# Performance work log

Hardware: AMD Instinct MI355X
Metric: run time of the kernel (lower is better)

The kernel has to match this reference:

```python
import jax, jax.numpy as jnp
import numpy as np

P_DROP = 0.25
DROP_KEY_SEED = 42  # fixed seed makes dropout deterministic for baseline comparison


def setup_inputs() -> dict:
    key = jax.random.key(0)
    k1, k2, k3, k4 = jax.random.split(key, 4)
    B, S, D, DV = 16, 2048, 64, 512
    x1 = jax.random.normal(k1, (B, S, D), dtype=jnp.float32)   # queries [B,S,64]
    m = jax.random.normal(k2, (D, DV), dtype=jnp.float32)      # [64,512]
    n = jax.random.normal(k3, (S, DV), dtype=jnp.float32)      # [S,512]
    q = jax.random.normal(k4, (S, DV), dtype=jnp.float32)      # values [S,512]
    return {"x1": x1, "m": m, "n": n, "q": q}


def reference(x1, m, n, q):
    scale = jnp.float32(1.0 / 64.0)  # hard-coded in original (not 1/sqrt(d))
    kT = jnp.matmul(m, n.T)                        # matmul5: [64, S]
    scores = jnp.matmul(x1, kT) * scale            # [B, S, S]
    probs = jax.nn.softmax(scores, axis=-1)        # softmax over last dim
    keep = jax.random.bernoulli(jax.random.key(DROP_KEY_SEED), 1.0 - P_DROP, probs.shape)
    probs = jnp.where(keep, probs / (1.0 - P_DROP), jnp.float32(0.0))  # dropout (train mode)
    return jnp.matmul(probs, q)                    # [B, S, DV]
```

## Files before the change

kernel.cpp:

```cpp
#include <hip/hip_runtime.h>
#include <hip/hip_bf16.h>


typedef short  s8v __attribute__((ext_vector_type(8)));
typedef float  f4v __attribute__((ext_vector_type(4)));

__device__ __forceinline__ unsigned short f2bf(float f) {
  unsigned int u = __float_as_uint(f);
  u += 0x7fffu + ((u >> 16) & 1u);
  return (unsigned short)(u >> 16);
}
__device__ __forceinline__ unsigned int pack_bf2(float a, float b) {
  __hip_bfloat162 h = __float22bfloat162_rn(float2{a, b});
  unsigned int u;
  __builtin_memcpy(&u, &h, 4);
  return u;
}

__device__ __forceinline__ unsigned int rotl(unsigned int x, unsigned int r) {
  return __builtin_amdgcn_alignbit(x, x, 32u - r);
}

__device__ __forceinline__ unsigned int jax_bits(unsigned int idx) {
  const unsigned int K0 = 0u, K1 = 42u, K2 = 0x1BD11BDAu ^ K0 ^ K1;
  unsigned int x0 = 0u, x1 = idx;
  x0 += K0; x1 += K1;
#define TF_R(r) { x0 += x1; x1 = rotl(x1, r); x1 ^= x0; }
  TF_R(13) TF_R(15) TF_R(26) TF_R(6)
  x0 += K1; x1 += K2 + 1u;
  TF_R(17) TF_R(29) TF_R(16) TF_R(24)
  x0 += K2; x1 += K0 + 2u;
  TF_R(13) TF_R(15) TF_R(26) TF_R(6)
  x0 += K0; x1 += K1 + 3u;
  TF_R(17) TF_R(29) TF_R(16) TF_R(24)
  x0 += K1; x1 += K2 + 4u;
  TF_R(13) TF_R(15) TF_R(26) TF_R(6)
  x0 += K2; x1 += K0 + 5u;
#undef TF_R
  return x0 ^ x1;
}

__device__ __forceinline__ f4v mfma16(s8v a, s8v b, f4v c) {
  return __builtin_amdgcn_mfma_f32_16x16x32_bf16(a, b, c, 0, 0, 0);
}

__global__ void prep_misc(const float* __restrict__ x1, const float* __restrict__ q,
                          unsigned short* __restrict__ Xhi,
                          unsigned short* __restrict__ qT) {
  const int blk = blockIdx.x;
  const int t = threadIdx.x;
  if (blk < 1024) {
    const int i = (blk * 256 + t) * 8;
    float4 a = *(const float4*)&x1[i];
    float4 b = *(const float4*)&x1[i + 4];
    ushort4 o0, o1;
    o0.x = f2bf(a.x); o0.y = f2bf(a.y); o0.z = f2bf(a.z); o0.w = f2bf(a.w);
    o1.x = f2bf(b.x); o1.y = f2bf(b.y); o1.z = f2bf(b.z); o1.w = f2bf(b.w);
    *(ushort4*)&Xhi[i] = o0;
    *(ushort4*)&Xhi[i + 4] = o1;
  } else {
    __shared__ unsigned short tile[64][65];
    const int bb = blk - 1024;
    const int s0 = (bb >> 3) * 64;
    const int d0 = (bb & 7) * 64;
#pragma unroll
    for (int k = 0; k < 16; ++k) {
      int lin = t + k * 256;
      int r = lin >> 6, c = lin & 63;
      tile[c][r] = f2bf(q[(size_t)(s0 + r) * 512 + d0 + c]);
    }
    __syncthreads();
#pragma unroll
    for (int k = 0; k < 16; ++k) {
      int lin = t + k * 256;
      int rr = lin >> 6, cc = lin & 63;
      qT[(size_t)(d0 + rr) * 2048 + s0 + cc] = tile[rr][cc];
    }
  }
}

__global__ __launch_bounds__(256) void build_k(const float* __restrict__ m,
                                               const float* __restrict__ n,
                                               unsigned short* __restrict__ Khi) {
  __shared__ float tile[32][65];
  const int t = threadIdx.x;
  const int d = t & 63;
  const int w = t >> 6;
  const int s0 = blockIdx.x * 16;
  const int ld_d = t >> 2;
  const int ld_c = (t & 3) * 8;
  float a0 = 0.f, a1 = 0.f, a2 = 0.f, a3 = 0.f;
  for (int c0 = 0; c0 < 512; c0 += 32) {
    __syncthreads();
    float4 va = *(const float4*)&m[ld_d * 512 + c0 + ld_c];
    float4 vb = *(const float4*)&m[ld_d * 512 + c0 + ld_c + 4];
    tile[ld_c + 0][ld_d] = va.x; tile[ld_c + 1][ld_d] = va.y;
    tile[ld_c + 2][ld_d] = va.z; tile[ld_c + 3][ld_d] = va.w;
    tile[ld_c + 4][ld_d] = vb.x; tile[ld_c + 5][ld_d] = vb.y;
    tile[ld_c + 6][ld_d] = vb.z; tile[ld_c + 7][ld_d] = vb.w;
    __syncthreads();
    const float* n0 = &n[(size_t)(s0 + w * 4 + 0) * 512 + c0];
    const float* n1 = &n[(size_t)(s0 + w * 4 + 1) * 512 + c0];
    const float* n2 = &n[(size_t)(s0 + w * 4 + 2) * 512 + c0];
    const float* n3 = &n[(size_t)(s0 + w * 4 + 3) * 512 + c0];
#pragma unroll
    for (int j = 0; j < 32; ++j) {
      float mv = tile[j][d];
      a0 = fmaf(mv, n0[j], a0); a1 = fmaf(mv, n1[j], a1);
      a2 = fmaf(mv, n2[j], a2); a3 = fmaf(mv, n3[j], a3);
    }
  }
  Khi[(s0 + w * 4 + 0) * 64 + d] = f2bf(a0 * 0.015625f);
  Khi[(s0 + w * 4 + 1) * 64 + d] = f2bf(a1 * 0.015625f);
  Khi[(s0 + w * 4 + 2) * 64 + d] = f2bf(a2 * 0.015625f);
  Khi[(s0 + w * 4 + 3) * 64 + d] = f2bf(a3 * 0.015625f);
}

__global__ __launch_bounds__(512, 4) void attn_main(
    const unsigned short* __restrict__ Xhi, const unsigned short* __restrict__ Khi,
    const unsigned short* __restrict__ qT, float* __restrict__ out) {
  __shared__ unsigned short Ps[2][64][152];
  __shared__ float rsum[2][64];

  const int tid  = threadIdx.x;
  const int wave = tid >> 6;
  const int lane = tid & 63;
  const int l15  = lane & 15;
  const int quad = lane >> 4;

  const int b    = blockIdx.x >> 5;
  const int row0 = (blockIdx.x & 31) * 64;

  const int qk_row = (wave & 3) * 16 + l15;
  const int qk_kg  = (wave >> 2) * 64;

  const size_t xg = ((size_t)(b * 2048 + row0 + qk_row)) * 64 + quad * 8;
  const s8v X0 = *(const s8v*)&Xhi[xg];
  const s8v X1 = *(const s8v*)&Xhi[xg + 32];

  f4v acc[4][4];
#pragma unroll
  for (int mt = 0; mt < 4; ++mt)
#pragma unroll
    for (int nt = 0; nt < 4; ++nt) acc[mt][nt] = f4v{0.f, 0.f, 0.f, 0.f};
  float rs = 0.f;

  const unsigned int idx_row =
      ((unsigned int)(b * 2048 + row0 + qk_row)) * 2048u;

  auto qktf_phase = [&](int it) {
    const int kt = it * 128;
    const int buf = it & 1;
    f4v cf[4];
#pragma unroll
    for (int nt = 0; nt < 4; ++nt) {
      const int key = kt + qk_kg + nt * 16 + l15;
      const s8v Ka = *(const s8v*)&Khi[key * 64 + quad * 8];
      const s8v Kb = *(const s8v*)&Khi[key * 64 + 32 + quad * 8];
      f4v c = {0.f, 0.f, 0.f, 0.f};
      c = mfma16(Ka, X0, c);
      cf[nt] = mfma16(Kb, X1, c);
    }
#pragma unroll
    for (int nt = 0; nt < 4; ++nt) {
      const unsigned int idx0 =
          idx_row + (unsigned int)(kt + qk_kg + nt * 16 + quad * 4);
      float p[4];
#pragma unroll
      for (int r = 0; r < 4; ++r) {
        float e = __expf(cf[nt][r]);
        rs += e;
        p[r] = (jax_bits(idx0 + r) < 0xC0000000u) ? e : 0.0f;
      }
      *(uint2*)&Ps[buf][(wave & 3) * 16 + l15][qk_kg + nt * 16 + quad * 4] =
          make_uint2(pack_bf2(p[0], p[1]), pack_bf2(p[2], p[3]));
    }
  };
  auto pv_phase = [&](int it) {
    const int kt = it * 128;
    const int buf = it & 1;
#pragma unroll
    for (int ks = 0; ks < 4; ++ks) {
      s8v Va[4];
#pragma unroll
      for (int mt = 0; mt < 4; ++mt)
        Va[mt] = *(const s8v*)&qT[(size_t)(wave * 64 + mt * 16 + l15) * 2048 +
                                  kt + ks * 32 + quad * 8];
#pragma unroll
      for (int nt = 0; nt < 4; ++nt) {
        const s8v Pb = *(const s8v*)&Ps[buf][nt * 16 + l15][ks * 32 + quad * 8];
#pragma unroll
        for (int mt = 0; mt < 4; ++mt)
          acc[mt][nt] = mfma16(Va[mt], Pb, acc[mt][nt]);
      }
    }
  };

  qktf_phase(0);
  __syncthreads();
  for (int it = 1; it < 16; ++it) {
    qktf_phase(it);
    pv_phase(it - 1);
    __syncthreads();
  }
  pv_phase(15);

  {
    float v = rs;
    v += __shfl_xor(v, 16);
    v += __shfl_xor(v, 32);
    if (quad == 0) rsum[wave >> 2][(wave & 3) * 16 + l15] = v;
  }
  __syncthreads();

#pragma unroll
  for (int nt = 0; nt < 4; ++nt) {
    const int rloc = nt * 16 + l15;
    const int row = row0 + rloc;
    const float inv = 1.0f / (0.75f * (rsum[0][rloc] + rsum[1][rloc]));
    const size_t base = ((size_t)(b * 2048 + row)) * 512 + wave * 64;
#pragma unroll
    for (int mt = 0; mt < 4; ++mt) {
      f4v v = acc[mt][nt];
      v[0] *= inv; v[1] *= inv; v[2] *= inv; v[3] *= inv;
      *(f4v*)&out[base + mt * 16 + quad * 4] = v;
    }
  }
}

extern "C" void kernel_launch(void* const* d_in, const int* in_sizes, int n_in,
                              void* d_out, int out_size, void* d_ws, size_t ws_size,
                              hipStream_t stream) {
  (void)in_sizes; (void)n_in; (void)out_size; (void)ws_size;
  const float* x1 = (const float*)d_in[0];
  const float* m  = (const float*)d_in[1];
  const float* n  = (const float*)d_in[2];
  const float* q  = (const float*)d_in[3];
  float* out = (float*)d_out;

  char* ws = (char*)d_ws;
  unsigned short* Khi = (unsigned short*)(ws + 0);
  unsigned short* Xhi = (unsigned short*)(ws + 262144);
  unsigned short* qT  = (unsigned short*)(ws + 4456448);

  prep_misc<<<1280, 256, 0, stream>>>(x1, q, Xhi, qT);
  build_k<<<128, 256, 0, stream>>>(m, n, Khi);
  attn_main<<<512, 512, 0, stream>>>(Xhi, Khi, qT, out);
}
```

Baseline: 348.3 us.

## Halve query rows per block, fold log2e into K scale, use exp2

Each block now handles 32 query rows instead of 64, so the grid doubles to 1024 blocks. Key columns are split four ways across waves, and the row sums are reduced over four partials. The K scale now includes log2(e), so the softmax can call the hardware exp2 directly, and the launch bounds ask for 6 waves per SIMD to raise occupancy. The trade-off is that each qT tile now feeds only 32 rows, so qT global reads and MFMA work per load lose reuse, and the extra blocks may hurt L2 traffic.

```diff
diff --git a/kernel.cpp b/kernel.cpp
--- a/kernel.cpp
+++ b/kernel.cpp
@@ -15,6 +15,14 @@
   unsigned int u;
   __builtin_memcpy(&u, &h, 4);
   return u;
+}
+
+__device__ __forceinline__ float fast_exp2(float x) {
+#if __has_builtin(__builtin_amdgcn_exp2f)
+  return __builtin_amdgcn_exp2f(x);
+#else
+  return exp2f(x);
+#endif
 }
 
 __device__ __forceinline__ unsigned int rotl(unsigned int x, unsigned int r) {
@@ -110,17 +118,18 @@
       a2 = fmaf(mv, n2[j], a2); a3 = fmaf(mv, n3[j], a3);
     }
   }
-  Khi[(s0 + w * 4 + 0) * 64 + d] = f2bf(a0 * 0.015625f);
-  Khi[(s0 + w * 4 + 1) * 64 + d] = f2bf(a1 * 0.015625f);
-  Khi[(s0 + w * 4 + 2) * 64 + d] = f2bf(a2 * 0.015625f);
-  Khi[(s0 + w * 4 + 3) * 64 + d] = f2bf(a3 * 0.015625f);
-}
-
-__global__ __launch_bounds__(512, 4) void attn_main(
+  const float SC = 0.022542109f;
+  Khi[(s0 + w * 4 + 0) * 64 + d] = f2bf(a0 * SC);
+  Khi[(s0 + w * 4 + 1) * 64 + d] = f2bf(a1 * SC);
+  Khi[(s0 + w * 4 + 2) * 64 + d] = f2bf(a2 * SC);
+  Khi[(s0 + w * 4 + 3) * 64 + d] = f2bf(a3 * SC);
+}
+
+__global__ __launch_bounds__(512, 6) void attn_main(
     const unsigned short* __restrict__ Xhi, const unsigned short* __restrict__ Khi,
     const unsigned short* __restrict__ qT, float* __restrict__ out) {
-  __shared__ unsigned short Ps[2][64][152];
-  __shared__ float rsum[2][64];
+  __shared__ unsigned short Ps[2][32][152];
+  __shared__ float rsum[4][32];
 
   const int tid  = threadIdx.x;
   const int wave = tid >> 6;
@@ -128,33 +137,33 @@
   const int l15  = lane & 15;
   const int quad = lane >> 4;
 
-  const int b    = blockIdx.x >> 5;
-  const int row0 = (blockIdx.x & 31) * 64;
-
-  const int qk_row = (wave & 3) * 16 + l15;
-  const int qk_kg  = (wave >> 2) * 64;
-
-  const size_t xg = ((size_t)(b * 2048 + row0 + qk_row)) * 64 + quad * 8;
+  const int b    = blockIdx.x >> 6;
+  const int row0 = (blockIdx.x & 63) * 32;
+
+  const int rowg = (wave & 1) * 16;
+  const int keyg = (wave >> 1) * 32;
+
+  const size_t xg = ((size_t)(b * 2048 + row0 + rowg + l15)) * 64 + quad * 8;
   const s8v X0 = *(const s8v*)&Xhi[xg];
   const s8v X1 = *(const s8v*)&Xhi[xg + 32];
 
-  f4v acc[4][4];
+  f4v acc[4][2];
 #pragma unroll
   for (int mt = 0; mt < 4; ++mt)
 #pragma unroll
-    for (int nt = 0; nt < 4; ++nt) acc[mt][nt] = f4v{0.f, 0.f, 0.f, 0.f};
+    for (int nt = 0; nt < 2; ++nt) acc[mt][nt] = f4v{0.f, 0.f, 0.f, 0.f};
   float rs = 0.f;
 
   const unsigned int idx_row =
-      ((unsigned int)(b * 2048 + row0 + qk_row)) * 2048u;
+      ((unsigned int)(b * 2048 + row0 + rowg + l15)) * 2048u;
 
   auto qktf_phase = [&](int it) {
     const int kt = it * 128;
     const int buf = it & 1;
-    f4v cf[4];
-#pragma unroll
-    for (int nt = 0; nt < 4; ++nt) {
-      const int key = kt + qk_kg + nt * 16 + l15;
+    f4v cf[2];
+#pragma unroll
+    for (int nt = 0; nt < 2; ++nt) {
+      const int key = kt + keyg + nt * 16 + l15;
       const s8v Ka = *(const s8v*)&Khi[key * 64 + quad * 8];
       const s8v Kb = *(const s8v*)&Khi[key * 64 + 32 + quad * 8];
       f4v c = {0.f, 0.f, 0.f, 0.f};
@@ -162,17 +171,17 @@
       cf[nt] = mfma16(Kb, X1, c);
     }
 #pragma unroll
-    for (int nt = 0; nt < 4; ++nt) {
+    for (int nt = 0; nt < 2; ++nt) {
       const unsigned int idx0 =
-          idx_row + (unsigned int)(kt + qk_kg + nt * 16 + quad * 4);
+          idx_row + (unsigned int)(kt + keyg + nt * 16 + quad * 4);
       float p[4];
 #pragma unroll
       for (int r = 0; r < 4; ++r) {
-        float e = __expf(cf[nt][r]);
+        float e = fast_exp2(cf[nt][r]);
         rs += e;
         p[r] = (jax_bits(idx0 + r) < 0xC0000000u) ? e : 0.0f;
       }
-      *(uint2*)&Ps[buf][(wave & 3) * 16 + l15][qk_kg + nt * 16 + quad * 4] =
+      *(uint2*)&Ps[buf][rowg + l15][keyg + nt * 16 + quad * 4] =
           make_uint2(pack_bf2(p[0], p[1]), pack_bf2(p[2], p[3]));
     }
   };
@@ -187,7 +196,7 @@
         Va[mt] = *(const s8v*)&qT[(size_t)(wave * 64 + mt * 16 + l15) * 2048 +
                                   kt + ks * 32 + quad * 8];
 #pragma unroll
-      for (int nt = 0; nt < 4; ++nt) {
+      for (int nt = 0; nt < 2; ++nt) {
         const s8v Pb = *(const s8v*)&Ps[buf][nt * 16 + l15][ks * 32 + quad * 8];
 #pragma unroll
         for (int mt = 0; mt < 4; ++mt)
@@ -209,15 +218,16 @@
     float v = rs;
     v += __shfl_xor(v, 16);
     v += __shfl_xor(v, 32);
-    if (quad == 0) rsum[wave >> 2][(wave & 3) * 16 + l15] = v;
+    if (quad == 0) rsum[wave >> 1][rowg + l15] = v;
   }
   __syncthreads();
 
 #pragma unroll
-  for (int nt = 0; nt < 4; ++nt) {
+  for (int nt = 0; nt < 2; ++nt) {
     const int rloc = nt * 16 + l15;
     const int row = row0 + rloc;
-    const float inv = 1.0f / (0.75f * (rsum[0][rloc] + rsum[1][rloc]));
+    const float inv = 1.0f / (0.75f * (rsum[0][rloc] + rsum[1][rloc] +
+                                       rsum[2][rloc] + rsum[3][rloc]));
     const size_t base = ((size_t)(b * 2048 + row)) * 512 + wave * 64;
 #pragma unroll
     for (int mt = 0; mt < 4; ++mt) {
@@ -245,5 +255,5 @@
 
   prep_misc<<<1280, 256, 0, stream>>>(x1, q, Xhi, qT);
   build_k<<<128, 256, 0, stream>>>(m, n, Khi);
-  attn_main<<<512, 512, 0, stream>>>(Xhi, Khi, qT, out);
-}
+  attn_main<<<1024, 512, 0, stream>>>(Xhi, Khi, qT, out);
+}
```

Result: slower. 459.3 us (+31.9%).
